# Kernel optimization log

Measured on AMD Instinct MI355X. Metric: run time of the kernel, lower is better.

The kernel has to match this reference:

```python
import jax, jax.numpy as jnp
import numpy as np

B, T, V, E, H, LAT, L = 2048, 120, 64, 128, 512, 256, 2


def setup_inputs() -> dict:
    key = jax.random.key(0)
    ks = jax.random.split(key, 16)
    s = 0.05  # weight init scale
    z = jax.random.normal(ks[0], (B, LAT), jnp.float32)
    target = jax.random.randint(ks[1], (B, T), 0, V)
    embed = (jax.random.normal(ks[2], (V, E), jnp.float32) * s).at[0].set(0.0)  # padding_idx=0
    fc_hidden_w = jax.random.normal(ks[3], (H * L, LAT), jnp.float32) * s
    fc_hidden_b = jax.random.normal(ks[4], (H * L,), jnp.float32) * s
    W_ih0 = jax.random.normal(ks[5], (3 * H, E + LAT), jnp.float32) * s
    W_hh0 = jax.random.normal(ks[6], (3 * H, H), jnp.float32) * s
    b_ih0 = jax.random.normal(ks[7], (3 * H,), jnp.float32) * s
    b_hh0 = jax.random.normal(ks[8], (3 * H,), jnp.float32) * s
    W_ih1 = jax.random.normal(ks[9], (3 * H, H), jnp.float32) * s
    W_hh1 = jax.random.normal(ks[10], (3 * H, H), jnp.float32) * s
    b_ih1 = jax.random.normal(ks[11], (3 * H,), jnp.float32) * s
    b_hh1 = jax.random.normal(ks[12], (3 * H,), jnp.float32) * s
    fc_out_w = jax.random.normal(ks[13], (V, H), jnp.float32) * s
    fc_out_b = jax.random.normal(ks[14], (V,), jnp.float32) * s
    return dict(z=z, target=target, embed=embed, fc_hidden_w=fc_hidden_w,
                fc_hidden_b=fc_hidden_b, W_ih0=W_ih0, W_hh0=W_hh0, b_ih0=b_ih0,
                b_hh0=b_hh0, W_ih1=W_ih1, W_hh1=W_hh1, b_ih1=b_ih1, b_hh1=b_hh1,
                fc_out_w=fc_out_w, fc_out_b=fc_out_b)


def _gru_cell(x, h, W_ih, W_hh, b_ih, b_hh):
    # torch GRU cell: r,z,n gate ordering
    gx = x @ W_ih.T + b_ih          # [B, 3H]
    gh = h @ W_hh.T + b_hh          # [B, 3H]
    xr, xz, xn = jnp.split(gx, 3, axis=-1)
    hr, hz, hn = jnp.split(gh, 3, axis=-1)
    r = jax.nn.sigmoid(xr + hr)
    u = jax.nn.sigmoid(xz + hz)
    n = jnp.tanh(xn + r * hn)
    return (1.0 - u) * n + u * h


def reference(z, target, embed, fc_hidden_w, fc_hidden_b, W_ih0, W_hh0, b_ih0,
              b_hh0, W_ih1, W_hh1, b_ih1, b_hh1, fc_out_w, fc_out_b):
    b, lat = z.shape
    t = target.shape[1]
    hd = W_hh0.shape[1]
    # initial hidden: fc_hidden(z).view(B, L, H) -> per-layer states
    hid = (z @ fc_hidden_w.T + fc_hidden_b).reshape(b, L, hd)
    h0, h1 = hid[:, 0, :], hid[:, 1, :]
    # teacher forcing with ratio 1.0: input_0 = token 1, input_t = target[:, t-1]
    tok = jnp.concatenate([jnp.ones((b, 1), target.dtype), target[:, :-1]], axis=1)
    # precompute per-step GRU inputs: [T, B, E+LAT]
    xs = jnp.concatenate(
        [embed[tok], jnp.broadcast_to(z[:, None, :], (b, t, lat))], axis=-1)
    xs = jnp.swapaxes(xs, 0, 1)

    def step(carry, x):
        h0, h1 = carry
        h0n = _gru_cell(x, h0, W_ih0, W_hh0, b_ih0, b_hh0)
        h1n = _gru_cell(h0n, h1, W_ih1, W_hh1, b_ih1, b_hh1)
        logits = h1n @ fc_out_w.T + fc_out_b
        return (h0n, h1n), logits

    _, out = jax.lax.scan(step, (h0, h1), xs)   # [T, B, V]
    return jnp.swapaxes(out, 0, 1)              # [B, T, V]
```

## Files before the change

kernel.cpp:

```cpp
#include <hip/hip_runtime.h>
#include <hip/hip_bf16.h>

#define DI __device__ __forceinline__

typedef short bf16x8 __attribute__((ext_vector_type(8)));
typedef float f32x4 __attribute__((ext_vector_type(4)));

constexpr int B_ = 2048, T_ = 120, V_ = 64, E_ = 128, H_ = 512, LAT_ = 256;
constexpr int H3 = 1536;

DI short f2b(float f) {
  union { __hip_bfloat16 h; short s; } u;
  u.h = __float2bfloat16(f);
  return u.s;
}
DI float b2f(short s) {
  union { unsigned u; float f; } x;
  x.u = (unsigned)(unsigned short)s << 16;
  return x.f;
}
DI float sigm(float x) { return 1.f / (1.f + __expf(-x)); }
DI float tanh_f(float x) {
  x = fminf(15.f, fmaxf(-15.f, x));
  float e = __expf(2.f * x);
  return (e - 1.f) / (e + 1.f);
}
DI float gru_one(float xr, float xz, float xn, float hr, float hz, float hn, float hp) {
  float r = sigm(xr + hr);
  float u = sigm(xz + hz);
  float nn = tanh_f(xn + r * hn);
  return (1.f - u) * nn + u * hp;
}
DI float gru_pre(float sr, float sz, float xn, float hn, float hp) {
  float r = sigm(sr);
  float u = sigm(sz);
  float nn = tanh_f(xn + r * hn);
  return (1.f - u) * nn + u * hp;
}

template <int ROWS, int BK, int NV>
DI void rs_load(const short* __restrict__ G, int row0, int K, int kk, bf16x8 (&v)[NV]) {
  constexpr int SLOTS = BK / 8;
  constexpr int RPP = 2048 / BK;
  static_assert(NV == ROWS / RPP, "NV mismatch");
  const int tid = threadIdx.x;
  const int rl = tid / SLOTS, sl = tid % SLOTS;
#pragma unroll
  for (int p = 0; p < NV; ++p)
    v[p] = *(const bf16x8*)(G + (size_t)(row0 + p * RPP + rl) * K + kk + sl * 8);
}
template <int ROWS, int BK, int NV>
DI void rs_write(char* __restrict__ lds, bf16x8 (&v)[NV]) {
  constexpr int SLOTS = BK / 8;
  constexpr int RPP = 2048 / BK;
  const int tid = threadIdx.x;
  const int rl = tid / SLOTS, sl = tid % SLOTS;
#pragma unroll
  for (int p = 0; p < NV; ++p) {
    int row = p * RPP + rl;
    *(bf16x8*)(lds + row * (SLOTS * 16) + ((sl ^ (row & (SLOTS - 1))) * 16)) = v[p];
  }
}
template <int BK>
DI bf16x8 fragL(const char* __restrict__ lds, int row, int kk) {
  return *(const bf16x8*)(lds + row * (BK * 2) + ((kk << 1) ^ ((row & (BK / 8 - 1)) << 4)));
}

DI void gemm_core(const short* __restrict__ A, const short* __restrict__ Bw,
                  int arow, int bcol, char* lds, f32x4 (&acc)[2][4]) {
  char* As[2] = {lds, lds + 8192};
  char* Bs[2] = {lds + 16384, lds + 32768};
  const int tid = threadIdx.x, lane = tid & 63, wid = tid >> 6;
  const int wm = wid >> 1, wn = wid & 1;
  const int r = lane & 15, ko = (lane >> 4) * 8;
  bf16x8 va[2], vb[4];
  rs_load<64, 64, 2>(A, arow, H_, 0, va);
  rs_load<128, 64, 4>(Bw, bcol, H_, 0, vb);
  rs_write<64, 64, 2>(As[0], va);
  rs_write<128, 64, 4>(Bs[0], vb);
  __syncthreads();
  int cur = 0;
  for (int c = 0; c < 8; ++c) {
    if (c < 7) {
      rs_load<64, 64, 2>(A, arow, H_, (c + 1) * 64, va);
      rs_load<128, 64, 4>(Bw, bcol, H_, (c + 1) * 64, vb);
    }
#pragma unroll
    for (int kh = 0; kh < 2; ++kh) {
      const int kkk = kh * 32 + ko;
      bf16x8 a[2], b[4];
#pragma unroll
      for (int i = 0; i < 2; ++i) a[i] = fragL<64>(As[cur], wm * 32 + i * 16 + r, kkk);
#pragma unroll
      for (int j = 0; j < 4; ++j) b[j] = fragL<64>(Bs[cur], wn * 64 + j * 16 + r, kkk);
#pragma unroll
      for (int i = 0; i < 2; ++i)
#pragma unroll
        for (int j = 0; j < 4; ++j)
          acc[i][j] = __builtin_amdgcn_mfma_f32_16x16x32_bf16(a[i], b[j], acc[i][j], 0, 0, 0);
    }
    if (c < 7) {
      rs_write<64, 64, 2>(As[cur ^ 1], va);
      rs_write<128, 64, 4>(Bs[cur ^ 1], vb);
    }
    __syncthreads();
    cur ^= 1;
  }
}

struct GArgs {
  const short* zgx; const short* egx; const int* target;
  float* h0f; float* h1f;
  short* h0b0; short* h0b1;
  short* h1b;
  short* p0;
  short* gx1a; short* gx1b;
  short* gh1;
  const short* Wb_hh0; const float* b_hh0;
  const short* Wb_ih1; const float* b_ih1;
  const short* Wb_hh1; const float* b_hh1;
  const short* Wb_out; const float* fc_out_b;
  float* out;
};

DI void unit_G0(const GArgs& a, int v, int t, char* smem) {
  const int tid = threadIdx.x, lane = tid & 63, wid = tid >> 6;
  const short* h0b_prev = ((t - 1) & 1) ? a.h0b1 : a.h0b0;
  const int mt = v / 12, nt = v % 12;
  const int arow = mt * 64, bcol = nt * 128;
  f32x4 acc[2][4] = {};
  gemm_core(h0b_prev, a.Wb_hh0, arow, bcol, smem, acc);
  const int wm = wid >> 1, wn = wid & 1;
  const int r0 = (lane >> 4) * 4, c0 = lane & 15;
  const int g = nt >> 2;
#pragma unroll
  for (int i = 0; i < 2; ++i)
#pragma unroll
    for (int j = 0; j < 4; ++j) {
      const int col = bcol + wn * 64 + j * 16 + c0;
      const int jj = col & 511;
      const float bv = a.b_hh0[col];
#pragma unroll
      for (int rr = 0; rr < 4; ++rr) {
        const int row = arow + wm * 32 + i * 16 + r0 + rr;
        const float val = acc[i][j][rr] + bv;
        const int tok = (t == 0) ? 1 : a.target[(size_t)row * T_ + (t - 1)];
        const float xv = b2f(a.zgx[(size_t)row * H3 + g * 512 + jj]) +
                         b2f(a.egx[(size_t)tok * H3 + g * 512 + jj]);
        short* pr = a.p0 + ((size_t)row * 4) * 512 + jj;
        if (g < 2) {
          pr[g * 512] = f2b(val + xv);
        } else {
          pr[2 * 512] = f2b(xv);
          pr[3 * 512] = f2b(val);
        }
      }
    }
}

DI void unit_X1(const GArgs& a, int v, int t, char* smem) {
  const int tid = threadIdx.x, lane = tid & 63, wid = tid >> 6;
  const short* h0b_prev = ((t - 1) & 1) ? a.h0b1 : a.h0b0;
  short* gxw = ((t - 1) & 1) ? a.gx1b : a.gx1a;
  const int mt = v / 12, nt = v % 12;
  const int arow = mt * 64, bcol = nt * 128;
  f32x4 acc[2][4] = {};
  gemm_core(h0b_prev, a.Wb_ih1, arow, bcol, smem, acc);
  const int wm = wid >> 1, wn = wid & 1;
  const int r0 = (lane >> 4) * 4, c0 = lane & 15;
#pragma unroll
  for (int i = 0; i < 2; ++i)
#pragma unroll
    for (int j = 0; j < 4; ++j) {
      const int col = bcol + wn * 64 + j * 16 + c0;
      const float bv = a.b_ih1[col];
#pragma unroll
      for (int rr = 0; rr < 4; ++rr)
        gxw[(size_t)(arow + wm * 32 + i * 16 + r0 + rr) * H3 + col] = f2b(acc[i][j][rr] + bv);
    }
}

DI void unit_G1(const GArgs& a, int v, int t, char* smem) {
  const int tid = threadIdx.x, lane = tid & 63, wid = tid >> 6;
  const int mt = v / 12, nt = v % 12;
  const int arow = mt * 64, bcol = nt * 128;
  f32x4 acc[2][4] = {};
  gemm_core(a.h1b, a.Wb_hh1, arow, bcol, smem, acc);
  const int wm = wid >> 1, wn = wid & 1;
  const int r0 = (lane >> 4) * 4, c0 = lane & 15;
#pragma unroll
  for (int i = 0; i < 2; ++i)
#pragma unroll
    for (int j = 0; j < 4; ++j) {
      const int col = bcol + wn * 64 + j * 16 + c0;
      const float bv = a.b_hh1[col];
#pragma unroll
      for (int rr = 0; rr < 4; ++rr)
        a.gh1[(size_t)(arow + wm * 32 + i * 16 + r0 + rr) * H3 + col] = f2b(acc[i][j][rr] + bv);
    }
}

DI void unit_P1(const GArgs& a, int v, int t, char* smem) {
  short* sh = (short*)smem;
  const short* gxr = (t & 1) ? a.gx1b : a.gx1a;
  const int tid = threadIdx.x;
  const int row0 = v * 16;
  const int tlog = t - 2;
#pragma unroll 1
  for (int c = 0; c < 4; ++c) {
    int f = c * 2048 + tid * 8;
    int rl = f >> 9, j = f & 511;
    int row = row0 + rl;
    const short* gx = gxr + (size_t)row * H3 + j;
    const short* gh = a.gh1 + (size_t)row * H3 + j;
    float* hf = a.h1f + (size_t)row * H_ + j;
    bf16x8 xr = *(const bf16x8*)(gx);
    bf16x8 xz = *(const bf16x8*)(gx + H_);
    bf16x8 xn = *(const bf16x8*)(gx + 2 * H_);
    bf16x8 hr = *(const bf16x8*)(gh);
    bf16x8 hz = *(const bf16x8*)(gh + H_);
    bf16x8 hn = *(const bf16x8*)(gh + 2 * H_);
    float4 hp0 = *(const float4*)(hf);
    float4 hp1 = *(const float4*)(hf + 4);
    float hp[8] = {hp0.x, hp0.y, hp0.z, hp0.w, hp1.x, hp1.y, hp1.z, hp1.w};
    float hv[8];
    bf16x8 ov;
#pragma unroll
    for (int e = 0; e < 8; ++e) {
      hv[e] = gru_one(b2f(xr[e]), b2f(xz[e]), b2f(xn[e]),
                      b2f(hr[e]), b2f(hz[e]), b2f(hn[e]), hp[e]);
      ov[e] = f2b(hv[e]);
    }
    *(float4*)(hf) = make_float4(hv[0], hv[1], hv[2], hv[3]);
    *(float4*)(hf + 4) = make_float4(hv[4], hv[5], hv[6], hv[7]);
    *(bf16x8*)(a.h1b + (size_t)row * H_ + j) = ov;
    *(bf16x8*)(&sh[rl * 520 + j]) = ov;
  }
  __syncthreads();
  const int lane = tid & 63, w = tid >> 6;
  const int c0 = lane & 15, ko = (lane >> 4) * 8;
  f32x4 acc = {};
  const short* wb = a.Wb_out + (size_t)(w * 16 + c0) * H_ + ko;
  const short* ap = &sh[c0 * 520 + ko];
#pragma unroll
  for (int m = 0; m < 16; ++m) {
    bf16x8 av = *(const bf16x8*)(ap + m * 32);
    bf16x8 bw = *(const bf16x8*)(wb + m * 32);
    acc = __builtin_amdgcn_mfma_f32_16x16x32_bf16(av, bw, acc, 0, 0, 0);
  }
  const int r0 = (lane >> 4) * 4;
  const int col = w * 16 + c0;
  const float bv = a.fc_out_b[col];
#pragma unroll
  for (int rr = 0; rr < 4; ++rr) {
    int brow = row0 + r0 + rr;
    a.out[((size_t)brow * T_ + tlog) * V_ + col] = acc[rr] + bv;
  }
}

DI void unit_Dp(const GArgs& a, int v, int t) {
  short* h0b_new = (t & 1) ? a.h0b1 : a.h0b0;
  const int tid = threadIdx.x;
  const int row0 = v * 16;
#pragma unroll 1
  for (int it = 0; it < 4; ++it) {
    int w = it * 256 + tid;
    int rl = w >> 6, jb = w & 63;
    int row = row0 + rl, j = jb * 8;
    const short* pr = a.p0 + ((size_t)row * 4) * 512 + j;
    bf16x8 sr = *(const bf16x8*)(pr);
    bf16x8 sz = *(const bf16x8*)(pr + 512);
    bf16x8 xn = *(const bf16x8*)(pr + 1024);
    bf16x8 hn = *(const bf16x8*)(pr + 1536);
    float* hf = a.h0f + (size_t)row * H_ + j;
    float4 hp0 = *(const float4*)(hf);
    float4 hp1 = *(const float4*)(hf + 4);
    float hp[8] = {hp0.x, hp0.y, hp0.z, hp0.w, hp1.x, hp1.y, hp1.z, hp1.w};
    float hv[8];
    bf16x8 ov;
#pragma unroll
    for (int e = 0; e < 8; ++e) {
      hv[e] = gru_pre(b2f(sr[e]), b2f(sz[e]), b2f(xn[e]), b2f(hn[e]), hp[e]);
      ov[e] = f2b(hv[e]);
    }
    *(float4*)(hf) = make_float4(hv[0], hv[1], hv[2], hv[3]);
    *(float4*)(hf + 4) = make_float4(hv[4], hv[5], hv[6], hv[7]);
    *(bf16x8*)(h0b_new + (size_t)row * H_ + j) = ov;
  }
}

__global__ __launch_bounds__(256) void k_A(GArgs a, int t) {
  extern __shared__ char smem[];
  const int u = blockIdx.x;
  if (u < 384) {
    if (t < T_) unit_G0(a, u, t, smem);
  } else if (u < 640) {
    if (t >= 1 && t <= T_) unit_X1(a, u - 384, t, smem);
  } else {
    if (t >= 2) unit_P1(a, u - 640, t, smem);
  }
}

__global__ __launch_bounds__(256) void k_C(GArgs a, int t) {
  extern __shared__ char smem[];
  const int u = blockIdx.x;
  if (u < 128) {
    if (t < T_) unit_Dp(a, u, t);
  } else if (u < 256) {
    if (t >= 1 && t <= T_) unit_X1(a, 256 + (u - 128), t, smem);
  } else {
    if (t >= 1 && t <= T_) unit_G1(a, u - 256, t, smem);
  }
}

template <int MI, int NJ>
DI void gemm_wave_global(const short* __restrict__ A, const short* __restrict__ B,
                         const int K, const int arow, const int bcol,
                         f32x4 (&acc)[MI][NJ]) {
  const int lane = threadIdx.x & 63;
  const int r = lane & 15, ko = (lane >> 4) * 8;
  const short* Ap = A + (size_t)(arow + r) * K + ko;
  const short* Bp = B + (size_t)(bcol + r) * K + ko;
  for (int kk = 0; kk < K; kk += 32) {
    bf16x8 a[MI], b[NJ];
#pragma unroll
    for (int i = 0; i < MI; ++i) a[i] = *(const bf16x8*)(Ap + (size_t)i * 16 * K + kk);
#pragma unroll
    for (int j = 0; j < NJ; ++j) b[j] = *(const bf16x8*)(Bp + (size_t)j * 16 * K + kk);
#pragma unroll
    for (int i = 0; i < MI; ++i)
#pragma unroll
      for (int j = 0; j < NJ; ++j)
        acc[i][j] = __builtin_amdgcn_mfma_f32_16x16x32_bf16(a[i], b[j], acc[i][j], 0, 0, 0);
  }
}
template <int MI, int NJ>
DI void epi_store_bf16(short* __restrict__ C, const float* __restrict__ bias,
                       const int N, const int arow, const int bcol, f32x4 (&acc)[MI][NJ]) {
  const int lane = threadIdx.x & 63;
  const int r0 = (lane >> 4) * 4, c0 = lane & 15;
#pragma unroll
  for (int i = 0; i < MI; ++i)
#pragma unroll
    for (int j = 0; j < NJ; ++j) {
      int col = bcol + j * 16 + c0;
      float bv = bias[col];
#pragma unroll
      for (int rr = 0; rr < 4; ++rr)
        C[(size_t)(arow + i * 16 + r0 + rr) * N + col] = f2b(acc[i][j][rr] + bv);
    }
}

__global__ __launch_bounds__(256) void k_prep0(
    const float* __restrict__ W_hh0, const float* __restrict__ W_ih1,
    const float* __restrict__ W_hh1, const float* __restrict__ fc_out_w,
    const float* __restrict__ W_ih0, const float* __restrict__ fc_hidden_w,
    const float* __restrict__ z,
    short* Wb_hh0, short* Wb_ih1, short* Wb_hh1, short* Wb_out,
    short* Wb_ih0z, short* Wb_fch, short* z_b) {
  const int n1 = H3 * H_;
  const int n2 = V_ * H_;
  const int n3 = H3 * LAT_;
  const int n4 = (2 * H_) * LAT_;
  const int n5 = B_ * LAT_;
  const int total = n1 * 3 + n2 + n3 + n4 + n5;
  for (int i = blockIdx.x * blockDim.x + threadIdx.x; i < total;
       i += gridDim.x * blockDim.x) {
    int idx = i;
    if (idx < n1) { Wb_hh0[idx] = f2b(W_hh0[idx]); continue; }
    idx -= n1;
    if (idx < n1) { Wb_ih1[idx] = f2b(W_ih1[idx]); continue; }
    idx -= n1;
    if (idx < n1) { Wb_hh1[idx] = f2b(W_hh1[idx]); continue; }
    idx -= n1;
    if (idx < n2) { Wb_out[idx] = f2b(fc_out_w[idx]); continue; }
    idx -= n2;
    if (idx < n3) {
      int n = idx >> 8, k = idx & 255;
      Wb_ih0z[idx] = f2b(W_ih0[(size_t)n * (E_ + LAT_) + E_ + k]);
      continue;
    }
    idx -= n3;
    if (idx < n4) { Wb_fch[idx] = f2b(fc_hidden_w[idx]); continue; }
    idx -= n4;
    z_b[idx] = f2b(z[idx]);
  }
}

__global__ __launch_bounds__(256) void k_prep_emb(const float* __restrict__ embed,
                                                  const float* __restrict__ W_ih0,
                                                  short* __restrict__ egx) {
  __shared__ float er[E_];
  int v = blockIdx.x;
  for (int e = threadIdx.x; e < E_; e += blockDim.x) er[e] = embed[(size_t)v * E_ + e];
  __syncthreads();
  for (int n = threadIdx.x; n < H3; n += blockDim.x) {
    const float* w = W_ih0 + (size_t)n * (E_ + LAT_);
    float acc = 0.f;
#pragma unroll 8
    for (int e = 0; e < E_; ++e) acc += er[e] * w[e];
    egx[(size_t)v * H3 + n] = f2b(acc);
  }
}

__global__ __launch_bounds__(256) void k_prep1(
    const short* __restrict__ z_b, const short* __restrict__ Wb_ih0z,
    const short* __restrict__ Wb_fch, const float* __restrict__ b_ih0,
    const float* __restrict__ fc_hidden_b,
    short* zgx, float* h0f, float* h1f, short* h0b_init, short* h1b) {
  const int bid = blockIdx.x;
  const int mtile = bid / 20, ntile = bid % 20;
  const int tid = threadIdx.x, lane = tid & 63, wid = tid >> 6;
  const int wm = wid >> 1, wn = wid & 1;
  const int arow = mtile * 128 + wm * 64;
  f32x4 acc[4][4] = {};
  if (ntile < 12) {
    int bcol = ntile * 128 + wn * 64;
    gemm_wave_global<4, 4>(z_b, Wb_ih0z, LAT_, arow, bcol, acc);
    epi_store_bf16<4, 4>(zgx, b_ih0, H3, arow, bcol, acc);
  } else {
    int bcol = (ntile - 12) * 128 + wn * 64;
    gemm_wave_global<4, 4>(z_b, Wb_fch, LAT_, arow, bcol, acc);
    const int r0 = (lane >> 4) * 4, c0 = lane & 15;
#pragma unroll
    for (int i = 0; i < 4; ++i)
#pragma unroll
      for (int j = 0; j < 4; ++j) {
        int col = bcol + j * 16 + c0;
        float bv = fc_hidden_b[col];
#pragma unroll
        for (int rr = 0; rr < 4; ++rr) {
          int row = arow + i * 16 + r0 + rr;
          float v = acc[i][j][rr] + bv;
          if (col < H_) {
            h0f[(size_t)row * H_ + col] = v;
            h0b_init[(size_t)row * H_ + col] = f2b(v);
          } else {
            h1f[(size_t)row * H_ + (col - H_)] = v;
            h1b[(size_t)row * H_ + (col - H_)] = f2b(v);
          }
        }
      }
  }
}

extern "C" void kernel_launch(void* const* d_in, const int* in_sizes, int n_in,
                              void* d_out, int out_size, void* d_ws, size_t ws_size,
                              hipStream_t stream) {
  const float* z           = (const float*)d_in[0];
  const int*   target      = (const int*)d_in[1];
  const float* embed       = (const float*)d_in[2];
  const float* fc_hidden_w = (const float*)d_in[3];
  const float* fc_hidden_b = (const float*)d_in[4];
  const float* W_ih0       = (const float*)d_in[5];
  const float* W_hh0       = (const float*)d_in[6];
  const float* b_ih0       = (const float*)d_in[7];
  const float* b_hh0       = (const float*)d_in[8];
  const float* W_ih1       = (const float*)d_in[9];
  const float* W_hh1       = (const float*)d_in[10];
  const float* b_ih1       = (const float*)d_in[11];
  const float* b_hh1       = (const float*)d_in[12];
  const float* fc_out_w    = (const float*)d_in[13];
  const float* fc_out_b    = (const float*)d_in[14];
  float* out = (float*)d_out;

  char* ws = (char*)d_ws;
  size_t off = 0;
  auto alloc = [&](size_t bytes) -> void* {
    off = (off + 255) & ~(size_t)255;
    void* p = ws + off;
    off += bytes;
    return p;
  };
  float* h0f    = (float*)alloc((size_t)B_ * H_ * 4);
  float* h1f    = (float*)alloc((size_t)B_ * H_ * 4);
  short* h0b0   = (short*)alloc((size_t)B_ * H_ * 2);
  short* h0b1   = (short*)alloc((size_t)B_ * H_ * 2);
  short* h1b    = (short*)alloc((size_t)B_ * H_ * 2);
  short* p0     = (short*)alloc((size_t)B_ * 4 * H_ * 2);
  short* gx1a   = (short*)alloc((size_t)B_ * H3 * 2);
  short* gx1b   = (short*)alloc((size_t)B_ * H3 * 2);
  short* gh1    = (short*)alloc((size_t)B_ * H3 * 2);
  short* zgx    = (short*)alloc((size_t)B_ * H3 * 2);
  short* egx    = (short*)alloc((size_t)V_ * H3 * 2);
  short* Wb_hh0 = (short*)alloc((size_t)H3 * H_ * 2);
  short* Wb_ih1 = (short*)alloc((size_t)H3 * H_ * 2);
  short* Wb_hh1 = (short*)alloc((size_t)H3 * H_ * 2);
  short* Wb_out = (short*)alloc((size_t)V_ * H_ * 2);
  short* Wb_ih0z= (short*)alloc((size_t)H3 * LAT_ * 2);
  short* Wb_fch = (short*)alloc((size_t)2 * H_ * LAT_ * 2);
  short* z_b    = (short*)alloc((size_t)B_ * LAT_ * 2);
  if (off > ws_size) return;

  k_prep0<<<2048, 256, 0, stream>>>(W_hh0, W_ih1, W_hh1, fc_out_w, W_ih0, fc_hidden_w,
                                    z, Wb_hh0, Wb_ih1, Wb_hh1, Wb_out, Wb_ih0z, Wb_fch, z_b);
  k_prep_emb<<<64, 256, 0, stream>>>(embed, W_ih0, egx);
  k_prep1<<<320, 256, 0, stream>>>(z_b, Wb_ih0z, Wb_fch, b_ih0, fc_hidden_b,
                                   zgx, h0f, h1f, h0b1, h1b);

  GArgs a;
  a.zgx = zgx; a.egx = egx; a.target = target;
  a.h0f = h0f; a.h1f = h1f;
  a.h0b0 = h0b0; a.h0b1 = h0b1;
  a.h1b = h1b; a.p0 = p0;
  a.gx1a = gx1a; a.gx1b = gx1b; a.gh1 = gh1;
  a.Wb_hh0 = Wb_hh0; a.b_hh0 = b_hh0;
  a.Wb_ih1 = Wb_ih1; a.b_ih1 = b_ih1;
  a.Wb_hh1 = Wb_hh1; a.b_hh1 = b_hh1;
  a.Wb_out = Wb_out; a.fc_out_b = fc_out_b;
  a.out = out;

  for (int t = 0; t <= T_ + 1; ++t) {
    k_A<<<768, 256, 49152, stream>>>(a, t);
    if (t <= T_) k_C<<<640, 256, 49152, stream>>>(a, t);
  }
}
```

Measured before the change: 4.604 ms.

## Fuse layer-0 GRU gate epilogue into hh0 GEMM and rebalance kernel schedule

The layer-0 hidden GEMM now computes all three gates (r, z, n) for a 32-row by 128-column slice inside one block. It then applies the GRU update in the epilogue and writes h0 directly, which removes the p0 staging buffer and the separate Dp elementwise pass. All X1 tiles move into k_A, and k_C now runs only G1, re-tiled to 32-row tiles across 768 blocks. Each G0F block computes three GEMMs in sequence and G1 tiles are smaller, which lowers per-block reuse and may leave the kernels unbalanced.

```diff
diff --git a/kernel.cpp b/kernel.cpp
--- a/kernel.cpp
+++ b/kernel.cpp
@@ -28,12 +28,6 @@
 DI float gru_one(float xr, float xz, float xn, float hr, float hz, float hn, float hp) {
   float r = sigm(xr + hr);
   float u = sigm(xz + hz);
-  float nn = tanh_f(xn + r * hn);
-  return (1.f - u) * nn + u * hp;
-}
-DI float gru_pre(float sr, float sz, float xn, float hn, float hp) {
-  float r = sigm(sr);
-  float u = sigm(sz);
   float nn = tanh_f(xn + r * hn);
   return (1.f - u) * nn + u * hp;
 }
@@ -108,12 +102,50 @@
   }
 }
 
+DI void gemm32(const short* __restrict__ A, const short* __restrict__ Bw,
+               int arow, int brow0, char* lds, f32x4 (&acc)[4]) {
+  char* As[2] = {lds, lds + 4096};
+  char* Bs[2] = {lds + 8192, lds + 24576};
+  const int tid = threadIdx.x, lane = tid & 63, wid = tid >> 6;
+  const int wm = wid >> 1, wn = wid & 1;
+  const int r = lane & 15, ko = (lane >> 4) * 8;
+  bf16x8 va[1], vb[4];
+  rs_load<32, 64, 1>(A, arow, H_, 0, va);
+  rs_load<128, 64, 4>(Bw, brow0, H_, 0, vb);
+  rs_write<32, 64, 1>(As[0], va);
+  rs_write<128, 64, 4>(Bs[0], vb);
+  __syncthreads();
+  int cur = 0;
+  for (int c = 0; c < 8; ++c) {
+    if (c < 7) {
+      rs_load<32, 64, 1>(A, arow, H_, (c + 1) * 64, va);
+      rs_load<128, 64, 4>(Bw, brow0, H_, (c + 1) * 64, vb);
+    }
+#pragma unroll
+    for (int kh = 0; kh < 2; ++kh) {
+      const int kkk = kh * 32 + ko;
+      bf16x8 af = fragL<64>(As[cur], wm * 16 + r, kkk);
+      bf16x8 b[4];
+#pragma unroll
+      for (int j = 0; j < 4; ++j) b[j] = fragL<64>(Bs[cur], wn * 64 + j * 16 + r, kkk);
+#pragma unroll
+      for (int j = 0; j < 4; ++j)
+        acc[j] = __builtin_amdgcn_mfma_f32_16x16x32_bf16(af, b[j], acc[j], 0, 0, 0);
+    }
+    if (c < 7) {
+      rs_write<32, 64, 1>(As[cur ^ 1], va);
+      rs_write<128, 64, 4>(Bs[cur ^ 1], vb);
+    }
+    __syncthreads();
+    cur ^= 1;
+  }
+}
+
 struct GArgs {
   const short* zgx; const short* egx; const int* target;
   float* h0f; float* h1f;
   short* h0b0; short* h0b1;
   short* h1b;
-  short* p0;
   short* gx1a; short* gx1b;
   short* gh1;
   const short* Wb_hh0; const float* b_hh0;
@@ -123,39 +155,38 @@
   float* out;
 };
 
-DI void unit_G0(const GArgs& a, int v, int t, char* smem) {
-  const int tid = threadIdx.x, lane = tid & 63, wid = tid >> 6;
+DI void unit_G0F(const GArgs& a, int v, int t, char* smem) {
   const short* h0b_prev = ((t - 1) & 1) ? a.h0b1 : a.h0b0;
-  const int mt = v / 12, nt = v % 12;
-  const int arow = mt * 64, bcol = nt * 128;
-  f32x4 acc[2][4] = {};
-  gemm_core(h0b_prev, a.Wb_hh0, arow, bcol, smem, acc);
+  short* h0b_new = (t & 1) ? a.h0b1 : a.h0b0;
+  const int mt = v >> 2, ns = v & 3;
+  const int arow = mt * 32, jb = ns * 128;
+  f32x4 acc[3][4] = {};
+#pragma unroll 1
+  for (int g = 0; g < 3; ++g)
+    gemm32(h0b_prev, a.Wb_hh0, arow, g * 512 + jb, smem, acc[g]);
+  const int lane = threadIdx.x & 63, wid = threadIdx.x >> 6;
   const int wm = wid >> 1, wn = wid & 1;
-  const int r0 = (lane >> 4) * 4, c0 = lane & 15;
-  const int g = nt >> 2;
-#pragma unroll
-  for (int i = 0; i < 2; ++i)
-#pragma unroll
-    for (int j = 0; j < 4; ++j) {
-      const int col = bcol + wn * 64 + j * 16 + c0;
-      const int jj = col & 511;
-      const float bv = a.b_hh0[col];
-#pragma unroll
-      for (int rr = 0; rr < 4; ++rr) {
-        const int row = arow + wm * 32 + i * 16 + r0 + rr;
-        const float val = acc[i][j][rr] + bv;
-        const int tok = (t == 0) ? 1 : a.target[(size_t)row * T_ + (t - 1)];
-        const float xv = b2f(a.zgx[(size_t)row * H3 + g * 512 + jj]) +
-                         b2f(a.egx[(size_t)tok * H3 + g * 512 + jj]);
-        short* pr = a.p0 + ((size_t)row * 4) * 512 + jj;
-        if (g < 2) {
-          pr[g * 512] = f2b(val + xv);
-        } else {
-          pr[2 * 512] = f2b(xv);
-          pr[3 * 512] = f2b(val);
-        }
-      }
-    }
+  const int q = lane >> 4, c0 = lane & 15;
+#pragma unroll
+  for (int j = 0; j < 4; ++j) {
+    const int jj = jb + wn * 64 + j * 16 + c0;
+    const float br = a.b_hh0[jj], bz = a.b_hh0[512 + jj], bn = a.b_hh0[1024 + jj];
+#pragma unroll
+    for (int rr = 0; rr < 4; ++rr) {
+      const int row = arow + wm * 16 + q * 4 + rr;
+      const int tok = (t == 0) ? 1 : a.target[(size_t)row * T_ + (t - 1)];
+      const short* zp = a.zgx + (size_t)row * H3 + jj;
+      const short* ep = a.egx + (size_t)tok * H3 + jj;
+      const float xr = b2f(zp[0]) + b2f(ep[0]);
+      const float xz = b2f(zp[512]) + b2f(ep[512]);
+      const float xn = b2f(zp[1024]) + b2f(ep[1024]);
+      const float hp = a.h0f[(size_t)row * H_ + jj];
+      const float h = gru_one(xr, xz, xn, acc[0][j][rr] + br, acc[1][j][rr] + bz,
+                              acc[2][j][rr] + bn, hp);
+      a.h0f[(size_t)row * H_ + jj] = h;
+      h0b_new[(size_t)row * H_ + jj] = f2b(h);
+    }
+  }
 }
 
 DI void unit_X1(const GArgs& a, int v, int t, char* smem) {
@@ -181,23 +212,21 @@
 }
 
 DI void unit_G1(const GArgs& a, int v, int t, char* smem) {
-  const int tid = threadIdx.x, lane = tid & 63, wid = tid >> 6;
   const int mt = v / 12, nt = v % 12;
-  const int arow = mt * 64, bcol = nt * 128;
-  f32x4 acc[2][4] = {};
-  gemm_core(a.h1b, a.Wb_hh1, arow, bcol, smem, acc);
+  const int arow = mt * 32, bcol = nt * 128;
+  f32x4 acc[4] = {};
+  gemm32(a.h1b, a.Wb_hh1, arow, bcol, smem, acc);
+  const int lane = threadIdx.x & 63, wid = threadIdx.x >> 6;
   const int wm = wid >> 1, wn = wid & 1;
-  const int r0 = (lane >> 4) * 4, c0 = lane & 15;
-#pragma unroll
-  for (int i = 0; i < 2; ++i)
-#pragma unroll
-    for (int j = 0; j < 4; ++j) {
-      const int col = bcol + wn * 64 + j * 16 + c0;
-      const float bv = a.b_hh1[col];
-#pragma unroll
-      for (int rr = 0; rr < 4; ++rr)
-        a.gh1[(size_t)(arow + wm * 32 + i * 16 + r0 + rr) * H3 + col] = f2b(acc[i][j][rr] + bv);
-    }
+  const int q = lane >> 4, c0 = lane & 15;
+#pragma unroll
+  for (int j = 0; j < 4; ++j) {
+    const int col = bcol + wn * 64 + j * 16 + c0;
+    const float bv = a.b_hh1[col];
+#pragma unroll
+    for (int rr = 0; rr < 4; ++rr)
+      a.gh1[(size_t)(arow + wm * 16 + q * 4 + rr) * H3 + col] = f2b(acc[j][rr] + bv);
+  }
 }
 
 DI void unit_P1(const GArgs& a, int v, int t, char* smem) {
@@ -258,44 +287,13 @@
   }
 }
 
-DI void unit_Dp(const GArgs& a, int v, int t) {
-  short* h0b_new = (t & 1) ? a.h0b1 : a.h0b0;
-  const int tid = threadIdx.x;
-  const int row0 = v * 16;
-#pragma unroll 1
-  for (int it = 0; it < 4; ++it) {
-    int w = it * 256 + tid;
-    int rl = w >> 6, jb = w & 63;
-    int row = row0 + rl, j = jb * 8;
-    const short* pr = a.p0 + ((size_t)row * 4) * 512 + j;
-    bf16x8 sr = *(const bf16x8*)(pr);
-    bf16x8 sz = *(const bf16x8*)(pr + 512);
-    bf16x8 xn = *(const bf16x8*)(pr + 1024);
-    bf16x8 hn = *(const bf16x8*)(pr + 1536);
-    float* hf = a.h0f + (size_t)row * H_ + j;
-    float4 hp0 = *(const float4*)(hf);
-    float4 hp1 = *(const float4*)(hf + 4);
-    float hp[8] = {hp0.x, hp0.y, hp0.z, hp0.w, hp1.x, hp1.y, hp1.z, hp1.w};
-    float hv[8];
-    bf16x8 ov;
-#pragma unroll
-    for (int e = 0; e < 8; ++e) {
-      hv[e] = gru_pre(b2f(sr[e]), b2f(sz[e]), b2f(xn[e]), b2f(hn[e]), hp[e]);
-      ov[e] = f2b(hv[e]);
-    }
-    *(float4*)(hf) = make_float4(hv[0], hv[1], hv[2], hv[3]);
-    *(float4*)(hf + 4) = make_float4(hv[4], hv[5], hv[6], hv[7]);
-    *(bf16x8*)(h0b_new + (size_t)row * H_ + j) = ov;
-  }
-}
-
 __global__ __launch_bounds__(256) void k_A(GArgs a, int t) {
   extern __shared__ char smem[];
   const int u = blockIdx.x;
-  if (u < 384) {
-    if (t < T_) unit_G0(a, u, t, smem);
+  if (u < 256) {
+    if (t < T_) unit_G0F(a, u, t, smem);
   } else if (u < 640) {
-    if (t >= 1 && t <= T_) unit_X1(a, u - 384, t, smem);
+    if (t >= 1 && t <= T_) unit_X1(a, u - 256, t, smem);
   } else {
     if (t >= 2) unit_P1(a, u - 640, t, smem);
   }
@@ -303,14 +301,7 @@
 
 __global__ __launch_bounds__(256) void k_C(GArgs a, int t) {
   extern __shared__ char smem[];
-  const int u = blockIdx.x;
-  if (u < 128) {
-    if (t < T_) unit_Dp(a, u, t);
-  } else if (u < 256) {
-    if (t >= 1 && t <= T_) unit_X1(a, 256 + (u - 128), t, smem);
-  } else {
-    if (t >= 1 && t <= T_) unit_G1(a, u - 256, t, smem);
-  }
+  unit_G1(a, blockIdx.x, t, smem);
 }
 
 template <int MI, int NJ>
@@ -477,7 +468,6 @@
   short* h0b0   = (short*)alloc((size_t)B_ * H_ * 2);
   short* h0b1   = (short*)alloc((size_t)B_ * H_ * 2);
   short* h1b    = (short*)alloc((size_t)B_ * H_ * 2);
-  short* p0     = (short*)alloc((size_t)B_ * 4 * H_ * 2);
   short* gx1a   = (short*)alloc((size_t)B_ * H3 * 2);
   short* gx1b   = (short*)alloc((size_t)B_ * H3 * 2);
   short* gh1    = (short*)alloc((size_t)B_ * H3 * 2);
@@ -502,7 +492,7 @@
   a.zgx = zgx; a.egx = egx; a.target = target;
   a.h0f = h0f; a.h1f = h1f;
   a.h0b0 = h0b0; a.h0b1 = h0b1;
-  a.h1b = h1b; a.p0 = p0;
+  a.h1b = h1b;
   a.gx1a = gx1a; a.gx1b = gx1b; a.gh1 = gh1;
   a.Wb_hh0 = Wb_hh0; a.b_hh0 = b_hh0;
   a.Wb_ih1 = Wb_ih1; a.b_ih1 = b_ih1;
@@ -512,6 +502,6 @@
 
   for (int t = 0; t <= T_ + 1; ++t) {
     k_A<<<768, 256, 49152, stream>>>(a, t);
-    if (t <= T_) k_C<<<640, 256, 49152, stream>>>(a, t);
-  }
-}
+    if (t >= 1 && t <= T_) k_C<<<768, 256, 40960, stream>>>(a, t);
+  }
+}
```

Result: slower. 6.904 ms (+50.0%).
